# Kernel tuning notes

Measured on AMD Instinct MI355X. Metric: run time of the kernel, lower is better.

## Reference

```python
import jax, jax.numpy as jnp
import numpy as np

# graph metadata: 3 node types, 4 canonical etypes
NT_SRC = (0, 1, 1, 2)   # src ntype of each relation
NT_DST = (1, 0, 2, 1)   # dst ntype of each relation
GROUPS = {0: (1,), 1: (0, 3), 2: (2,)}  # relations sharing each dst ntype (in dict order)
NEG_SLOPE = 0.2
N_NODES, N_EDGES, IN_DIM = 50000, 200000, 256
HEADS, HID = 8, 32
REL_IN, REL_HID = 64, 32


def _leaky(x):
    return jax.nn.leaky_relu(x, NEG_SLOPE)


def _segment_softmax(e, seg, n):
    # numerically stable softmax over edges grouped by dst node
    m = jax.ops.segment_max(e, seg, num_segments=n)
    ex = jnp.exp(e - m[seg])
    s = jax.ops.segment_sum(ex, seg, num_segments=n)
    return ex / s[seg]


def setup_inputs() -> dict:
    key = jax.random.key(0)
    ks = jax.random.split(key, 12)
    w = 0.05  # xavier-like scale
    feat = jax.random.normal(ks[0], (4, N_NODES, IN_DIM), jnp.float32)
    rel_emb = jax.random.normal(ks[1], (4, REL_IN), jnp.float32)
    node_W = jax.random.normal(ks[2], (3, IN_DIM, HEADS * HID), jnp.float32) * w
    rel_W = jax.random.normal(ks[3], (4, REL_IN, HEADS * 2 * HID), jnp.float32) * w
    res_W = jax.random.normal(ks[4], (3, IN_DIM, HEADS * HID), jnp.float32) * w
    res_b = jnp.zeros((3, HEADS * HID), jnp.float32)
    res_alpha = jax.random.normal(ks[5], (3,), jnp.float32)
    cross_attn = jax.random.normal(ks[6], (4, HEADS, HID), jnp.float32) * w
    prop_W = jax.random.normal(ks[7], (4, REL_IN, HEADS * REL_HID), jnp.float32) * w
    prop_b = jnp.zeros((4, HEADS * REL_HID), jnp.float32)
    src_idx = jax.random.randint(ks[8], (4, N_EDGES), 0, N_NODES, jnp.int32)
    dst_idx = jax.random.randint(ks[9], (4, N_EDGES), 0, N_NODES, jnp.int32)
    return dict(feat=feat, rel_emb=rel_emb, node_W=node_W, rel_W=rel_W,
                res_W=res_W, res_b=res_b, res_alpha=res_alpha,
                cross_attn=cross_attn, prop_W=prop_W, prop_b=prop_b,
                src_idx=src_idx, dst_idx=dst_idx)


def reference(feat, rel_emb, node_W, rel_W, res_W, res_b, res_alpha,
              cross_attn, prop_W, prop_b, src_idx, dst_idx):
    R, N, _ = feat.shape
    H, D = HEADS, HID
    conv_out = []
    for r in range(R):  # fixed small set of relations
        s, d = NT_SRC[r], NT_DST[r]
        # RelationGraphConv (dropout is identity in eval)
        fsrc = (feat[r] @ node_W[s]).reshape(N, H, D)
        fdst = (feat[r] @ node_W[d]).reshape(N, H, D)
        ra = (rel_emb[r] @ rel_W[r]).reshape(H, 2 * D)
        e_dst = (fdst * ra[:, :D]).sum(-1)           # (N, H)
        e_src = (fsrc * ra[:, D:]).sum(-1)           # (N, H)
        e = _leaky(e_src[src_idx[r]] + e_dst[dst_idx[r]])  # (E, H)
        a = _segment_softmax(e, dst_idx[r], N)       # edge softmax per dst node
        msg = fsrc[src_idx[r]] * a[:, :, None]       # (E, H, D)
        out = jax.ops.segment_sum(msg, dst_idx[r], num_segments=N)
        out = jax.nn.relu(out.reshape(N, H * D))
        # residual gate
        alpha = jax.nn.sigmoid(res_alpha[d])
        out = out * alpha + (feat[r] @ res_W[d] + res_b[d]) * (1.0 - alpha)
        conv_out.append(out)
    # RelationCrossing over relations sharing the dst ntype
    node_out = []
    for r in range(R):
        group = GROUPS[NT_DST[r]]
        if len(group) == 1:
            node_out.append(conv_out[group[0]])
        else:
            stacked = jnp.stack([conv_out[g] for g in group], 0).reshape(len(group), N, H, D)
            att = _leaky((stacked * cross_attn[r]).sum(-1, keepdims=True))  # (Rg, N, H, 1)
            att = jax.nn.softmax(att, axis=0)
            node_out.append((stacked * att).sum(0).reshape(N, H * D))
    node_out = jnp.stack(node_out, 0)                # (4, N, H*D)
    # relation embedding propagation
    rel_out = jnp.einsum('ri,rio->ro', rel_emb, prop_W) + prop_b  # (4, H*rel_hid)
    return node_out, rel_out
```

## Files before the change

### kernel.cpp

```cpp
#include <hip/hip_runtime.h>
#include <hip/hip_bf16.h>
#include <stdint.h>

typedef unsigned int u32;
typedef unsigned short u16;
typedef short short8 __attribute__((ext_vector_type(8)));
typedef float f32x4 __attribute__((ext_vector_type(4)));
typedef __attribute__((address_space(1))) const u32 gu32;
typedef __attribute__((address_space(3))) u32 lu32;

#define NN 50000
#define NE 200000
#define WCT 576

__device__ __forceinline__ float leaky(float x){ return x >= 0.f ? x : 0.2f*x; }
__device__ __forceinline__ float bf2f(u16 u){ return __uint_as_float(((u32)u)<<16); }
__device__ __forceinline__ u16 f2bf(float f){
    u32 u = __float_as_uint(f);
    u32 r = (u + 0x7fffu + ((u>>16)&1u)) >> 16;
    return (u16)r;
}
__device__ __forceinline__ u32 pack_bf2(float a, float b){
    return __builtin_amdgcn_perm(__float_as_uint(b), __float_as_uint(a), 0x07060302u);
}
__device__ __forceinline__ int nt_src(int r){ return (r==0)?0:((r==3)?2:1); }
__device__ __forceinline__ int nt_dst(int r){ return (r==1)?0:((r==2)?2:1); }

__global__ void k_ra(const float* __restrict__ rel_emb, const float* __restrict__ rel_W,
                     float* __restrict__ ra){
    int r = blockIdx.x;
    for (int j = threadIdx.x; j < 512; j += blockDim.x){
        float acc = 0.f;
        for (int i = 0; i < 64; i++) acc += rel_emb[r*64+i] * rel_W[(r*64+i)*512 + j];
        ra[r*512 + j] = acc;
    }
}

__global__ void k_wcat(const float* __restrict__ node_W, const float* __restrict__ res_W,
                       const float* __restrict__ ra, u16* __restrict__ WcatS){
    int g = blockIdx.x*blockDim.x + threadIdx.x;
    if (g >= 4*WCT*256) return;
    int r = g/147456; int rem = g%147456;
    int tile = rem/16384; int rem2 = rem%16384;
    int kc = rem2/512; int rem3 = rem2%512;
    int nrow = rem3>>3; int off = rem3&7;
    int n = tile*64 + nrow;
    int k = kc*8 + off;
    int s = nt_src(r), d = nt_dst(r);
    float v;
    if (n < 256) v = node_W[(s*256+k)*256 + n];
    else if (n < 512) v = res_W[(d*256+k)*256 + (n-256)];
    else if (n < 520){
        int h = n-512; float a = 0.f;
        for (int dd = 0; dd < 32; dd++) a += node_W[(s*256+k)*256 + h*32+dd] * ra[r*512 + h*64+32+dd];
        v = a;
    } else if (n < 528){
        int h = n-520; float a = 0.f;
        for (int dd = 0; dd < 32; dd++) a += node_W[(d*256+k)*256 + h*32+dd] * ra[r*512 + h*64+dd];
        v = a;
    } else v = 0.f;
    WcatS[g] = f2bf(v);
}

__launch_bounds__(256)
__global__ void k_gemm(const float* __restrict__ feat, const u16* __restrict__ WcatS,
                       const float* __restrict__ res_b,
                       u16* __restrict__ fsrc, u16* __restrict__ resb,
                       float* __restrict__ e_comb){
    __shared__ uint4 lsB[4096];
    __shared__ u16  cst[64*72];
    const short8* lsB8 = (const short8*)lsB;

    int r = blockIdx.y;
    int row0 = blockIdx.x*64;
    const float* A = feat + (size_t)r*NN*256;
    const u16*   W = WcatS + (size_t)r*9*16384;

    int t = threadIdx.x;
    int w = t>>6, l = t&63;
    int wm = (w>>1)*32, wn = (w&1)*32;
    int li = l & 15, lg = l >> 4;

    short8 afr[2][8];
    #pragma unroll
    for (int mt = 0; mt < 2; mt++){
        int grow = row0 + wm + mt*16 + li; if (grow > NN-1) grow = NN-1;
        const float* ap = A + (size_t)grow*256 + lg*8;
        #pragma unroll
        for (int kk = 0; kk < 8; kk++){
            float4 x = *(const float4*)(ap + kk*32);
            float4 y = *(const float4*)(ap + kk*32 + 4);
            short8 f;
            ((u32*)&f)[0] = pack_bf2(x.x, x.y);
            ((u32*)&f)[1] = pack_bf2(x.z, x.w);
            ((u32*)&f)[2] = pack_bf2(y.x, y.y);
            ((u32*)&f)[3] = pack_bf2(y.z, y.w);
            afr[mt][kk] = f;
        }
    }

    #pragma unroll
    for (int i = 0; i < 8; i++){
        int chunk = w*512 + i*64 + l;
        __builtin_amdgcn_global_load_lds((gu32*)(W + (size_t)chunk*8),
                                         (lu32*)((char*)lsB + (w*512 + i*64)*16), 16, 0, 0);
    }
    __syncthreads();

    int d = nt_dst(r);
    int orow = t>>2, oq = t&3;
    int ogrow = row0 + orow;
    size_t onidx = (size_t)r*NN + ogrow;

    for (int T = 0; T < 8; T++){
        int cur = T & 1;
        {
            const u16* tb = W + (size_t)(T+1)*16384;
            char* lb = (char*)lsB + (cur^1)*32768;
            #pragma unroll
            for (int i = 0; i < 8; i++){
                int chunk = w*512 + i*64 + l;
                __builtin_amdgcn_global_load_lds((gu32*)(tb + (size_t)chunk*8),
                                                 (lu32*)(lb + (w*512 + i*64)*16), 16, 0, 0);
            }
        }
        f32x4 acc[2][2] = {};
        #pragma unroll
        for (int kk = 0; kk < 8; kk++){
            short8 bfr[2];
            #pragma unroll
            for (int nt = 0; nt < 2; nt++)
                bfr[nt] = lsB8[cur*2048 + (kk*4+lg)*64 + wn + nt*16 + li];
            #pragma unroll
            for (int mt = 0; mt < 2; mt++)
                #pragma unroll
                for (int nt = 0; nt < 2; nt++)
                    acc[mt][nt] = __builtin_amdgcn_mfma_f32_16x16x32_bf16(afr[mt][kk], bfr[nt], acc[mt][nt], 0,0,0);
        }
        float bias[2] = {0.f, 0.f};
        if (T >= 4){
            bias[0] = res_b[d*256 + (T-4)*64 + wn + li];
            bias[1] = res_b[d*256 + (T-4)*64 + wn + 16 + li];
        }
        #pragma unroll
        for (int mt = 0; mt < 2; mt++)
            #pragma unroll
            for (int nt = 0; nt < 2; nt++)
                #pragma unroll
                for (int qq = 0; qq < 4; qq++)
                    cst[(wm + mt*16 + lg*4 + qq)*72 + wn + nt*16 + li] = f2bf(acc[mt][nt][qq] + bias[nt]);
        __syncthreads();
        if (ogrow < NN){
            u16* dst = (T < 4) ? (fsrc + onidx*256 + T*64) : (resb + onidx*256 + (T-4)*64);
            const uint4* src = (const uint4*)(cst + orow*72 + oq*16);
            uint4* dq = (uint4*)(dst + oq*16);
            dq[0] = src[0];
            dq[1] = src[1];
        }
        __syncthreads();
    }

    if (wn == 0){
        f32x4 acc[2] = {};
        #pragma unroll
        for (int kk = 0; kk < 8; kk++){
            short8 bfr = lsB8[(kk*4+lg)*64 + li];
            #pragma unroll
            for (int mt = 0; mt < 2; mt++)
                acc[mt] = __builtin_amdgcn_mfma_f32_16x16x32_bf16(afr[mt][kk], bfr, acc[mt], 0,0,0);
        }
        #pragma unroll
        for (int mt = 0; mt < 2; mt++)
            #pragma unroll
            for (int qq = 0; qq < 4; qq++){
                int row = row0 + wm + mt*16 + lg*4 + qq;
                if (row < NN)
                    e_comb[((size_t)r*NN + row)*16 + li] = acc[mt][qq];
            }
    }
}


__global__ void k_count(const int* __restrict__ dst_idx, u32* __restrict__ cnt){
    int r = blockIdx.y; int e = blockIdx.x*256 + threadIdx.x;
    if (e >= NE) return;
    atomicAdd(&cnt[r*NN + dst_idx[r*NE+e]], 1u);
}

__global__ void k_scan1(const u32* __restrict__ cnt, u32* __restrict__ bsum){
    int r = blockIdx.y, b = blockIdx.x;
    int i = b*256 + threadIdx.x;
    u32 v = (i < NN) ? cnt[r*NN+i] : 0u;
    #pragma unroll
    for (int off = 1; off < 64; off <<= 1) v += __shfl_xor(v, off, 64);
    __shared__ u32 wsum[4];
    int lane = threadIdx.x & 63, w = threadIdx.x >> 6;
    if (lane == 0) wsum[w] = v;
    __syncthreads();
    if (threadIdx.x == 0) bsum[r*256 + b] = wsum[0]+wsum[1]+wsum[2]+wsum[3];
}

__device__ __forceinline__ u32 block_scan_incl(u32 v){
    __shared__ u32 wsum[4];
    int lane = threadIdx.x & 63, w = threadIdx.x >> 6;
    #pragma unroll
    for (int off = 1; off < 64; off <<= 1){
        u32 t = __shfl_up(v, off, 64);
        if (lane >= off) v += t;
    }
    if (lane == 63) wsum[w] = v;
    __syncthreads();
    u32 add = 0;
    #pragma unroll
    for (int k = 0; k < 4; k++) if (k < w) add += wsum[k];
    return v + add;
}

__global__ void k_scan2(u32* __restrict__ bsum){
    int r = blockIdx.x;
    u32 v = bsum[r*256 + threadIdx.x];
    u32 incl = block_scan_incl(v);
    bsum[r*256 + threadIdx.x] = incl - v;
}

__global__ void k_scan3(const u32* __restrict__ cnt, const u32* __restrict__ bsum,
                        u32* __restrict__ row_ptr){
    int r = blockIdx.y, b = blockIdx.x;
    int i = b*256 + threadIdx.x;
    u32 v = (i < NN) ? cnt[r*NN+i] : 0u;
    u32 incl = block_scan_incl(v);
    if (i < NN) row_ptr[r*(NN+1) + i + 1] = bsum[r*256 + b] + incl;
    if (b == 0 && threadIdx.x == 0) row_ptr[r*(NN+1)] = 0u;
}

__global__ void k_scatter(const int* __restrict__ src_idx, const int* __restrict__ dst_idx,
                          const float* __restrict__ e_comb,
                          const u32* __restrict__ row_ptr, u32* __restrict__ cnt2,
                          u32* __restrict__ src_pack, float* __restrict__ e_pack){
    int r = blockIdx.y; int e = blockIdx.x*256 + threadIdx.x;
    if (e >= NE) return;
    int s = src_idx[r*NE+e], d = dst_idx[r*NE+e];
    u32 pos = row_ptr[r*(NN+1)+d] + atomicAdd(&cnt2[r*NN+d], 1u);
    src_pack[r*NE + pos] = (u32)s;
    const float* es = e_comb + (size_t)(r*NN+s)*16;
    const float* ed = e_comb + (size_t)(r*NN+d)*16 + 8;
    float* ep = e_pack + ((size_t)(r*NE)+pos)*8;
    #pragma unroll
    for (int h = 0; h < 8; h++) ep[h] = leaky(es[h] + ed[h]);
}

__launch_bounds__(256)
__global__ void k_aggx(const u32* __restrict__ row_ptr, const u32* __restrict__ src_pack,
                       const float* __restrict__ e_pack, const u16* __restrict__ fsrc,
                       const u16* __restrict__ resb, const float* __restrict__ res_alpha,
                       const float* __restrict__ cross_attn, float* __restrict__ out){
    __shared__ float cbuf[2][256];
    __shared__ float dots[4][8];

    int n = blockIdx.x;
    int r = threadIdx.x >> 6;
    int l = threadIdx.x & 63;
    int h = l >> 3;

    u32 p0 = row_ptr[r*(NN+1)+n];
    u32 p1 = row_ptr[r*(NN+1)+n+1];
    int deg = (int)(p1 - p0);

    float m = -1e30f, s = 0.f;
    for (int i = (l>>3); i < deg; i += 8){
        float e = e_pack[((size_t)(r*NE) + p0 + i)*8 + (l&7)];
        float mn = fmaxf(m, e);
        s = s*__expf(m - mn) + __expf(e - mn);
        m = mn;
    }
    #pragma unroll
    for (int msk = 8; msk < 64; msk <<= 1){
        float m2 = __shfl_xor(m, msk, 64);
        float s2 = __shfl_xor(s, msk, 64);
        float mn = fmaxf(m, m2);
        s = s*__expf(m - mn) + s2*__expf(m2 - mn);
        m = mn;
    }
    float mh = __shfl(m, h, 64);
    float sh = __shfl(s, h, 64);
    float inv_sh = 1.0f / sh;

    float a0=0.f, a1=0.f, a2=0.f, a3=0.f;
    const size_t ebase = (size_t)r*NE + p0;
    const u16* fbase = fsrc + (size_t)r*NN*256;
    for (int base = 0; base < deg; base += 64){
        int rem = deg - base; if (rem > 64) rem = 64;
        u32 my_src = 0;
        if (l < rem) my_src = src_pack[ebase + base + l];
        int i = 0;
        for (; i+2 <= rem; i += 2){
            u32 s0 = __shfl(my_src, i, 64);
            u32 s1 = __shfl(my_src, i+1, 64);
            float e0 = e_pack[(ebase + base + i)*8 + h];
            float e1 = e_pack[(ebase + base + i + 1)*8 + h];
            ushort4 f0 = *(const ushort4*)(fbase + (size_t)s0*256 + l*4);
            ushort4 f1 = *(const ushort4*)(fbase + (size_t)s1*256 + l*4);
            float w0 = __expf(e0 - mh)*inv_sh;
            float w1 = __expf(e1 - mh)*inv_sh;
            a0 += bf2f(f0.x)*w0 + bf2f(f1.x)*w1;
            a1 += bf2f(f0.y)*w0 + bf2f(f1.y)*w1;
            a2 += bf2f(f0.z)*w0 + bf2f(f1.z)*w1;
            a3 += bf2f(f0.w)*w0 + bf2f(f1.w)*w1;
        }
        if (i < rem){
            u32 s0 = __shfl(my_src, i, 64);
            float e0 = e_pack[(ebase + base + i)*8 + h];
            ushort4 f0 = *(const ushort4*)(fbase + (size_t)s0*256 + l*4);
            float w0 = __expf(e0 - mh)*inv_sh;
            a0 += bf2f(f0.x)*w0; a1 += bf2f(f0.y)*w0; a2 += bf2f(f0.z)*w0; a3 += bf2f(f0.w)*w0;
        }
    }

    int d = nt_dst(r);
    float alpha = 1.f/(1.f + __expf(-res_alpha[d]));
    float beta = 1.f - alpha;
    ushort4 rv = *(const ushort4*)(resb + ((size_t)r*NN+n)*256 + l*4);
    float c0 = fmaxf(a0,0.f)*alpha + bf2f(rv.x)*beta;
    float c1 = fmaxf(a1,0.f)*alpha + bf2f(rv.y)*beta;
    float c2 = fmaxf(a2,0.f)*alpha + bf2f(rv.z)*beta;
    float c3 = fmaxf(a3,0.f)*alpha + bf2f(rv.w)*beta;

    if (r == 1 || r == 2){
        float4 o = {c0, c1, c2, c3};
        *(float4*)(out + ((size_t)r*NN+n)*256 + l*4) = o;
    } else {
        int slot = (r == 0) ? 0 : 1;
        cbuf[slot][l*4+0] = c0; cbuf[slot][l*4+1] = c1;
        cbuf[slot][l*4+2] = c2; cbuf[slot][l*4+3] = c3;
        const float* ca0 = cross_attn;
        const float* ca3 = cross_attn + 3*256;
        float d0 = c0*ca0[l*4+0] + c1*ca0[l*4+1] + c2*ca0[l*4+2] + c3*ca0[l*4+3];
        float d3 = c0*ca3[l*4+0] + c1*ca3[l*4+1] + c2*ca3[l*4+2] + c3*ca3[l*4+3];
        #pragma unroll
        for (int msk = 1; msk < 8; msk <<= 1){
            d0 += __shfl_xor(d0, msk, 64);
            d3 += __shfl_xor(d3, msk, 64);
        }
        if ((l & 7) == 0){
            dots[slot*2+0][h] = d0;
            dots[slot*2+1][h] = d3;
        }
    }
    __syncthreads();
    if (r == 0 || r == 3){
        float g0 = (r == 0) ? dots[0][h] : dots[1][h];
        float g3 = (r == 0) ? dots[2][h] : dots[3][h];
        g0 = leaky(g0); g3 = leaky(g3);
        float mm = fmaxf(g0, g3);
        float w0 = __expf(g0-mm), w3 = __expf(g3-mm);
        float inv = 1.f/(w0+w3);
        w0 *= inv; w3 *= inv;
        float4 o;
        o.x = w0*cbuf[0][l*4+0] + w3*cbuf[1][l*4+0];
        o.y = w0*cbuf[0][l*4+1] + w3*cbuf[1][l*4+1];
        o.z = w0*cbuf[0][l*4+2] + w3*cbuf[1][l*4+2];
        o.w = w0*cbuf[0][l*4+3] + w3*cbuf[1][l*4+3];
        *(float4*)(out + ((size_t)r*NN+n)*256 + l*4) = o;
    }
}

__global__ void k_relout(const float* __restrict__ rel_emb, const float* __restrict__ prop_W,
                         const float* __restrict__ prop_b, float* __restrict__ out){
    int r = blockIdx.x; int o = threadIdx.x;
    float acc = prop_b[r*256 + o];
    for (int i = 0; i < 64; i++) acc += rel_emb[r*64+i] * prop_W[(r*64+i)*256 + o];
    out[(size_t)4*NN*256 + r*256 + o] = acc;
}

extern "C" void kernel_launch(void* const* d_in, const int* in_sizes, int n_in,
                              void* d_out, int out_size, void* d_ws, size_t ws_size,
                              hipStream_t stream){
    const float* feat      = (const float*)d_in[0];
    const float* rel_emb   = (const float*)d_in[1];
    const float* node_W    = (const float*)d_in[2];
    const float* rel_W     = (const float*)d_in[3];
    const float* res_W     = (const float*)d_in[4];
    const float* res_b     = (const float*)d_in[5];
    const float* res_alpha = (const float*)d_in[6];
    const float* cross_attn= (const float*)d_in[7];
    const float* prop_W    = (const float*)d_in[8];
    const float* prop_b    = (const float*)d_in[9];
    const int* src_idx     = (const int*)d_in[10];
    const int* dst_idx     = (const int*)d_in[11];
    float* out = (float*)d_out;

    char* ws = (char*)d_ws;
    u32*   cnt     = (u32*)  (ws);
    u32*   cnt2    = (u32*)  (ws + 800000);
    u32*   bsum    = (u32*)  (ws + 1600000);
    u32*   row_ptr = (u32*)  (ws + 1604096);
    float* ra      = (float*)(ws + 2404112);
    u16*   WcatS   = (u16*)  (ws + 2412304);
    float* e_comb  = (float*)(ws + 3591952);
    u32*   src_pack= (u32*)  (ws + 16391952);
    float* e_pack  = (float*)(ws + 19591952);
    u16*   fsrc    = (u16*)  (ws + 45191952);
    u16*   resb    = (u16*)  (ws + 147591952);

    hipMemsetAsync(cnt, 0, 1604096, stream);

    k_ra<<<4, 256, 0, stream>>>(rel_emb, rel_W, ra);
    k_wcat<<<(4*WCT*256)/256, 256, 0, stream>>>(node_W, res_W, ra, WcatS);
    dim3 gg((NN+63)/64, 4);
    k_gemm<<<gg, 256, 0, stream>>>(feat, WcatS, res_b, fsrc, resb, e_comb);

    dim3 geg((NE+255)/256, 4);
    k_count<<<geg, 256, 0, stream>>>(dst_idx, cnt);
    dim3 gsc((NN+255)/256, 4);
    k_scan1<<<gsc, 256, 0, stream>>>(cnt, bsum);
    k_scan2<<<4, 256, 0, stream>>>(bsum);
    k_scan3<<<gsc, 256, 0, stream>>>(cnt, bsum, row_ptr);
    k_scatter<<<geg, 256, 0, stream>>>(src_idx, dst_idx, e_comb, row_ptr, cnt2,
                                       src_pack, e_pack);
    k_aggx<<<NN, 256, 0, stream>>>(row_ptr, src_pack, e_pack, fsrc, resb,
                                   res_alpha, cross_attn, out);
    k_relout<<<4, 256, 0, stream>>>(rel_emb, prop_W, prop_b, out);
}
```

Measured before the change: 464.6 us.

## Precompute exp scores in scatter, drop max pass, unroll gather, nontemporal I/O

```diff
diff --git a/kernel.cpp b/kernel.cpp
--- a/kernel.cpp
+++ b/kernel.cpp
@@ -6,6 +6,7 @@
 typedef unsigned short u16;
 typedef short short8 __attribute__((ext_vector_type(8)));
 typedef float f32x4 __attribute__((ext_vector_type(4)));
+typedef unsigned short u16x4 __attribute__((ext_vector_type(4)));
 typedef __attribute__((address_space(1))) const u32 gu32;
 typedef __attribute__((address_space(3))) u32 lu32;
 
@@ -88,8 +89,8 @@
         const float* ap = A + (size_t)grow*256 + lg*8;
         #pragma unroll
         for (int kk = 0; kk < 8; kk++){
-            float4 x = *(const float4*)(ap + kk*32);
-            float4 y = *(const float4*)(ap + kk*32 + 4);
+            f32x4 x = __builtin_nontemporal_load((const f32x4*)(ap + kk*32));
+            f32x4 y = __builtin_nontemporal_load((const f32x4*)(ap + kk*32 + 4));
             short8 f;
             ((u32*)&f)[0] = pack_bf2(x.x, x.y);
             ((u32*)&f)[1] = pack_bf2(x.z, x.w);
@@ -242,11 +243,16 @@
     int s = src_idx[r*NE+e], d = dst_idx[r*NE+e];
     u32 pos = row_ptr[r*(NN+1)+d] + atomicAdd(&cnt2[r*NN+d], 1u);
     src_pack[r*NE + pos] = (u32)s;
-    const float* es = e_comb + (size_t)(r*NN+s)*16;
-    const float* ed = e_comb + (size_t)(r*NN+d)*16 + 8;
-    float* ep = e_pack + ((size_t)(r*NE)+pos)*8;
-    #pragma unroll
-    for (int h = 0; h < 8; h++) ep[h] = leaky(es[h] + ed[h]);
+    const f32x4* es = (const f32x4*)(e_comb + (size_t)(r*NN+s)*16);
+    const f32x4* ed = (const f32x4*)(e_comb + (size_t)(r*NN+d)*16 + 8);
+    f32x4 s0 = es[0], s1 = es[1], d0 = ed[0], d1 = ed[1];
+    f32x4 w0, w1;
+    w0.x = __expf(leaky(s0.x+d0.x)); w0.y = __expf(leaky(s0.y+d0.y));
+    w0.z = __expf(leaky(s0.z+d0.z)); w0.w = __expf(leaky(s0.w+d0.w));
+    w1.x = __expf(leaky(s1.x+d1.x)); w1.y = __expf(leaky(s1.y+d1.y));
+    w1.z = __expf(leaky(s1.z+d1.z)); w1.w = __expf(leaky(s1.w+d1.w));
+    f32x4* ep = (f32x4*)(e_pack + ((size_t)(r*NE)+pos)*8);
+    ep[0] = w0; ep[1] = w1;
 }
 
 __launch_bounds__(256)
@@ -266,24 +272,14 @@
     u32 p1 = row_ptr[r*(NN+1)+n+1];
     int deg = (int)(p1 - p0);
 
-    float m = -1e30f, s = 0.f;
-    for (int i = (l>>3); i < deg; i += 8){
-        float e = e_pack[((size_t)(r*NE) + p0 + i)*8 + (l&7)];
-        float mn = fmaxf(m, e);
-        s = s*__expf(m - mn) + __expf(e - mn);
-        m = mn;
-    }
-    #pragma unroll
-    for (int msk = 8; msk < 64; msk <<= 1){
-        float m2 = __shfl_xor(m, msk, 64);
-        float s2 = __shfl_xor(s, msk, 64);
-        float mn = fmaxf(m, m2);
-        s = s*__expf(m - mn) + s2*__expf(m2 - mn);
-        m = mn;
-    }
-    float mh = __shfl(m, h, 64);
+    float s = 0.f;
+    for (int i = (l>>3); i < deg; i += 8)
+        s += e_pack[((size_t)(r*NE) + p0 + i)*8 + (l&7)];
+    #pragma unroll
+    for (int msk = 8; msk < 64; msk <<= 1)
+        s += __shfl_xor(s, msk, 64);
     float sh = __shfl(s, h, 64);
-    float inv_sh = 1.0f / sh;
+    float inv_sh = (deg > 0) ? 1.0f / sh : 0.f;
 
     float a0=0.f, a1=0.f, a2=0.f, a3=0.f;
     const size_t ebase = (size_t)r*NE + p0;
@@ -293,25 +289,29 @@
         u32 my_src = 0;
         if (l < rem) my_src = src_pack[ebase + base + l];
         int i = 0;
-        for (; i+2 <= rem; i += 2){
+        for (; i+4 <= rem; i += 4){
             u32 s0 = __shfl(my_src, i, 64);
             u32 s1 = __shfl(my_src, i+1, 64);
-            float e0 = e_pack[(ebase + base + i)*8 + h];
-            float e1 = e_pack[(ebase + base + i + 1)*8 + h];
+            u32 s2 = __shfl(my_src, i+2, 64);
+            u32 s3 = __shfl(my_src, i+3, 64);
+            float ex0 = e_pack[(ebase + base + i)*8 + h];
+            float ex1 = e_pack[(ebase + base + i + 1)*8 + h];
+            float ex2 = e_pack[(ebase + base + i + 2)*8 + h];
+            float ex3 = e_pack[(ebase + base + i + 3)*8 + h];
             ushort4 f0 = *(const ushort4*)(fbase + (size_t)s0*256 + l*4);
             ushort4 f1 = *(const ushort4*)(fbase + (size_t)s1*256 + l*4);
-            float w0 = __expf(e0 - mh)*inv_sh;
-            float w1 = __expf(e1 - mh)*inv_sh;
-            a0 += bf2f(f0.x)*w0 + bf2f(f1.x)*w1;
-            a1 += bf2f(f0.y)*w0 + bf2f(f1.y)*w1;
-            a2 += bf2f(f0.z)*w0 + bf2f(f1.z)*w1;
-            a3 += bf2f(f0.w)*w0 + bf2f(f1.w)*w1;
-        }
-        if (i < rem){
+            ushort4 f2 = *(const ushort4*)(fbase + (size_t)s2*256 + l*4);
+            ushort4 f3 = *(const ushort4*)(fbase + (size_t)s3*256 + l*4);
+            float w0 = ex0*inv_sh, w1 = ex1*inv_sh, w2 = ex2*inv_sh, w3 = ex3*inv_sh;
+            a0 += bf2f(f0.x)*w0 + bf2f(f1.x)*w1 + bf2f(f2.x)*w2 + bf2f(f3.x)*w3;
+            a1 += bf2f(f0.y)*w0 + bf2f(f1.y)*w1 + bf2f(f2.y)*w2 + bf2f(f3.y)*w3;
+            a2 += bf2f(f0.z)*w0 + bf2f(f1.z)*w1 + bf2f(f2.z)*w2 + bf2f(f3.z)*w3;
+            a3 += bf2f(f0.w)*w0 + bf2f(f1.w)*w1 + bf2f(f2.w)*w2 + bf2f(f3.w)*w3;
+        }
+        for (; i < rem; i++){
             u32 s0 = __shfl(my_src, i, 64);
-            float e0 = e_pack[(ebase + base + i)*8 + h];
+            float w0 = e_pack[(ebase + base + i)*8 + h]*inv_sh;
             ushort4 f0 = *(const ushort4*)(fbase + (size_t)s0*256 + l*4);
-            float w0 = __expf(e0 - mh)*inv_sh;
             a0 += bf2f(f0.x)*w0; a1 += bf2f(f0.y)*w0; a2 += bf2f(f0.z)*w0; a3 += bf2f(f0.w)*w0;
         }
     }
@@ -319,15 +319,15 @@
     int d = nt_dst(r);
     float alpha = 1.f/(1.f + __expf(-res_alpha[d]));
     float beta = 1.f - alpha;
-    ushort4 rv = *(const ushort4*)(resb + ((size_t)r*NN+n)*256 + l*4);
+    u16x4 rv = __builtin_nontemporal_load((const u16x4*)(resb + ((size_t)r*NN+n)*256 + l*4));
     float c0 = fmaxf(a0,0.f)*alpha + bf2f(rv.x)*beta;
     float c1 = fmaxf(a1,0.f)*alpha + bf2f(rv.y)*beta;
     float c2 = fmaxf(a2,0.f)*alpha + bf2f(rv.z)*beta;
     float c3 = fmaxf(a3,0.f)*alpha + bf2f(rv.w)*beta;
 
     if (r == 1 || r == 2){
-        float4 o = {c0, c1, c2, c3};
-        *(float4*)(out + ((size_t)r*NN+n)*256 + l*4) = o;
+        f32x4 o = {c0, c1, c2, c3};
+        __builtin_nontemporal_store(o, (f32x4*)(out + ((size_t)r*NN+n)*256 + l*4));
     } else {
         int slot = (r == 0) ? 0 : 1;
         cbuf[slot][l*4+0] = c0; cbuf[slot][l*4+1] = c1;
@@ -355,12 +355,12 @@
         float w0 = __expf(g0-mm), w3 = __expf(g3-mm);
         float inv = 1.f/(w0+w3);
         w0 *= inv; w3 *= inv;
-        float4 o;
+        f32x4 o;
         o.x = w0*cbuf[0][l*4+0] + w3*cbuf[1][l*4+0];
         o.y = w0*cbuf[0][l*4+1] + w3*cbuf[1][l*4+1];
         o.z = w0*cbuf[0][l*4+2] + w3*cbuf[1][l*4+2];
         o.w = w0*cbuf[0][l*4+3] + w3*cbuf[1][l*4+3];
-        *(float4*)(out + ((size_t)r*NN+n)*256 + l*4) = o;
+        __builtin_nontemporal_store(o, (f32x4*)(out + ((size_t)r*NN+n)*256 + l*4));
     }
 }
 
```

New measurement: 446.3 us. -3.9%, faster.
